# Kernel tuning notes

Hardware: AMD Instinct MI355X
Metric: run time of the kernel (lower is better)

The kernel has to match this reference:

```python
import jax, jax.numpy as jnp
import numpy as np

_EPSILON = 1e-06


def _allocation(usage):
    """Freeness-based allocation: sort usage, exclusive cumprod, scatter back.

    usage: [B, M] in [0, 1]. Returns allocation weights [B, M].
    """
    usage = _EPSILON + (1.0 - _EPSILON) * usage
    nonusage = 1.0 - usage
    m = usage.shape[-1]
    sorted_nonusage, indices = jax.lax.top_k(nonusage, k=m)  # descending nonusage = ascending usage
    sorted_usage = 1.0 - sorted_nonusage
    # exclusive cumulative product along the sorted memory axis
    prod_sorted_usage = jnp.concatenate(
        [jnp.ones_like(sorted_usage[:, :1]),
         jnp.cumprod(sorted_usage, axis=1)[:, :-1]], axis=1)
    sorted_allocation = sorted_nonusage * prod_sorted_usage
    # invert the permutation and gather back to original slot order
    inverse_indices = jnp.argsort(indices, axis=1)
    return jnp.take_along_axis(sorted_allocation, inverse_indices, axis=1)


def _updated_usage(write_weights, free_gate, read_weights, prev_usage):
    """Freeness.__call__: usage after write then after read/free. [B, M]."""
    ww = jax.lax.stop_gradient(write_weights)
    # usage after write: increase toward 1 at written slots
    write_w = 1.0 - jnp.prod(1.0 - ww, axis=1)          # [B, M]
    usage = prev_usage + (1.0 - prev_usage) * write_w
    # usage after read: decrease where free_gate*read_weights is high
    free_read = free_gate[:, :, None] * read_weights      # [B, R, M]
    phi = jnp.prod(1.0 - free_read, axis=1)               # [B, M]
    return usage * phi


def _write_allocation_weights(usage, write_gates, num_writes):
    """Per-write-head allocation weights. Returns [B, num_writes, M]."""
    wg = write_gates[:, :, None]                          # [B, W, 1]
    allocs = []
    for i in range(num_writes):  # small fixed head count; sequential by construction
        a = _allocation(usage)
        allocs.append(a)
        usage = usage + (1.0 - usage) * wg[:, i, :] * a
    return jnp.stack(allocs, axis=1)


def setup_inputs() -> dict:
    key = jax.random.key(0)
    ks = jax.random.split(key, 5)
    B, W, R, M = 512, 4, 8, 16384
    return {
        "write_weights": jax.random.uniform(ks[0], (B, W, M), dtype=jnp.float32),
        "free_gate": jax.random.uniform(ks[1], (B, R), dtype=jnp.float32),
        "read_weights": jax.random.uniform(ks[2], (B, R, M), dtype=jnp.float32),
        "prev_usage": jax.random.uniform(ks[3], (B, M), dtype=jnp.float32),
        "write_gates": jax.random.uniform(ks[4], (B, W), dtype=jnp.float32),
        "num_writes": W,
    }


def reference(write_weights, free_gate, read_weights, prev_usage, write_gates, num_writes):
    usage = _updated_usage(write_weights, free_gate, read_weights, prev_usage)
    alloc = _write_allocation_weights(usage, write_gates, num_writes)
    return usage, alloc
```

## Files before the change

### kernel.cpp

```cpp
#include <hip/hip_runtime.h>
#include <stdint.h>

typedef unsigned long long u64;
typedef unsigned int u32;
typedef unsigned short u16;
typedef float f32x4 __attribute__((ext_vector_type(4)));

#define NBINS 512
#define CAP 256
#define POOLCAP 1024
#define LOG_CUT (-30.0f)
#define NT 1024
#define MWW 256

__device__ __forceinline__ int bucket_of(u32 nnbits) {
    u32 d = 0x3F800000u - nnbits;
    if (d == 0u) d = 1u;
    const int e = 31 - __builtin_clz(d);
    const u32 sub = (e >= 4) ? ((d >> (e - 4)) & 15u) : ((d << (4 - e)) & 15u);
    int v = (e << 4) | (int)sub;
    if (v > NBINS - 1) v = NBINS - 1;
    return (NBINS - 1) - v;
}

__device__ __forceinline__ void nt_store4(float* p, float4 v) {
    f32x4 nv;
    nv.x = v.x; nv.y = v.y; nv.z = v.z; nv.w = v.w;
    __builtin_nontemporal_store(nv, (f32x4*)p);
}

template <int TW, int TR>
__global__ __launch_bounds__(NT, 8)
void fused_kernel(const float* __restrict__ ww,
                  const float* __restrict__ fg,
                  const float* __restrict__ rw,
                  const float* __restrict__ prev,
                  const float* __restrict__ wgt,
                  float* __restrict__ out_usage,
                  float* __restrict__ out_alloc,
                  int B, int W, int R, int M)
{
    __shared__ u64   poolKey[POOLCAP];
    __shared__ float poolLg[POOLCAP];
    __shared__ u64   candKey[CAP];
    __shared__ float candLg[CAP];
    __shared__ u16   candPos[CAP];
    __shared__ float sPart[3][CAP];
    __shared__ u32   hC[NBINS];
    __shared__ float mB[NBINS];
    __shared__ u32   tc[16];
    __shared__ float twv[16];
    __shared__ int   misc[6];
    __shared__ u64   bmS[TW > 0 ? TW : 1][MWW];
    __shared__ u32   boS[TW > 0 ? TW : 1][MWW];
    __shared__ float valS[TW > 0 ? TW : 1][CAP];

    const int Wl = TW > 0 ? TW : W;
    const int Rl = TR > 0 ? TR : R;
    const int b = blockIdx.x;
    const int t = threadIdx.x;
    const int lane = t & 63;
    const int wid = t >> 6;

    const float C1 = (float)(1.0 - 1e-6);
    const float CE = 1e-6f;
    const size_t rowOff = (size_t)b * M;

    if (t < NBINS) {
        hC[t] = 0u;
        const int v = NBINS - 1 - t;
        const int e = v >> 4;
        const u32 sub = (u32)(v & 15);
        const int sh = e >= 4 ? e - 4 : 0;
        u64 dhi64 = ((u64)(17u + sub) << sh) + 1u;
        u32 dhi = dhi64 > 0x3F800000ull ? 0x3F800000u : (u32)dhi64;
        const float nnlo = __uint_as_float(0x3F800000u - dhi);
        float ueub = 1.0f - nnlo;
        ueub = ueub < 1e-38f ? 1e-38f : (ueub > 0.9999999f ? 0.9999999f : ueub);
        mB[t] = __log2f(ueub);
    }
    if (TW > 0 && t < TW * MWW) bmS[t >> 8][t & (MWW - 1)] = 0ull;
    if (t == 0) { misc[0] = 0; misc[3] = NBINS; }
    __syncthreads();

    {
        float frs[TR > 0 ? TR : 8];
        #pragma unroll
        for (int r = 0; r < Rl; ++r) frs[r] = fg[(size_t)b * Rl + r];

        for (int m = t * 4; m < M; m += NT * 4) {
            const float4 pv = *(const float4*)(prev + rowOff + m);
            float pr0 = 1.f, pr1 = 1.f, pr2 = 1.f, pr3 = 1.f;
            #pragma unroll
            for (int w = 0; w < Wl; ++w) {
                const float4 a = *(const float4*)(ww + ((size_t)b * Wl + w) * M + m);
                pr0 *= (1.0f - a.x); pr1 *= (1.0f - a.y);
                pr2 *= (1.0f - a.z); pr3 *= (1.0f - a.w);
            }
            float u0 = pv.x + (1.0f - pv.x) * (1.0f - pr0);
            float u1 = pv.y + (1.0f - pv.y) * (1.0f - pr1);
            float u2 = pv.z + (1.0f - pv.z) * (1.0f - pr2);
            float u3 = pv.w + (1.0f - pv.w) * (1.0f - pr3);
            float f0 = 1.f, f1 = 1.f, f2 = 1.f, f3 = 1.f;
            #pragma unroll
            for (int r = 0; r < Rl; ++r) {
                const float fr = frs[r];
                const float4 a = *(const float4*)(rw + ((size_t)b * Rl + r) * M + m);
                f0 *= (1.0f - fr * a.x); f1 *= (1.0f - fr * a.y);
                f2 *= (1.0f - fr * a.z); f3 *= (1.0f - fr * a.w);
            }
            float4 uo;
            uo.x = u0 * f0; uo.y = u1 * f1; uo.z = u2 * f2; uo.w = u3 * f3;
            *(float4*)(out_usage + rowOff + m) = uo;
            if (TW == 0) {
                const float4 z = make_float4(0.f, 0.f, 0.f, 0.f);
                for (int w = 0; w < Wl; ++w)
                    nt_store4(out_alloc + ((size_t)b * Wl + w) * M + m, z);
            }
            const float ua[4] = {uo.x, uo.y, uo.z, uo.w};
            #pragma unroll
            for (int j = 0; j < 4; ++j) {
                const float nn = 1.0f - (CE + C1 * ua[j]);
                atomicAdd(&hC[bucket_of(__float_as_uint(nn))], 1u);
            }
        }
    }
    __syncthreads();

    {
        const bool act = (t < NBINS);
        u32 sc = 0; int x = 0;
        if (act) {
            x = NBINS - 1 - t;
            sc = hC[x];
            #pragma unroll
            for (int off = 1; off < 64; off <<= 1) {
                const u32 oc = __shfl_up(sc, off);
                if (lane >= off) sc += oc;
            }
            if (lane == 63) tc[wid] = sc;
        }
        __syncthreads();
        if (act) {
            u32 ac = 0;
            for (int q = 0; q < wid; ++q) ac += tc[q];
            sc += ac;
            if (sc <= (u32)POOLCAP) atomicMin(&misc[3], x);
        }
    }
    __syncthreads();
    const int pc = misc[3];

    for (int m = t * 4; m < M; m += NT * 4) {
        const float4 uu = *(const float4*)(out_usage + rowOff + m);
        const float ua[4] = {uu.x, uu.y, uu.z, uu.w};
        #pragma unroll
        for (int j = 0; j < 4; ++j) {
            const float ue = CE + C1 * ua[j];
            const float nn = 1.0f - ue;
            const u32 nnbits = __float_as_uint(nn);
            const int bkt = bucket_of(nnbits);
            const bool pred = (bkt >= pc) && (pc < NBINS);
            const u64 mask = __ballot(pred);
            const int cnt = __popcll(mask);
            if (cnt) {
                int base = 0;
                if (lane == 0) base = atomicAdd(&misc[0], cnt);
                base = __shfl(base, 0);
                if (pred) {
                    const int pos = base + __popcll(mask & ((1ull << lane) - 1));
                    if (pos < POOLCAP) {
                        poolKey[pos] = (((u64)(~nnbits)) << 16) | (u64)(u32)(m + j);
                        poolLg[pos] = __log2f(ue);
                    }
                }
            }
        }
    }
    __syncthreads();
    int P = misc[0]; if (P > POOLCAP) P = POOLCAP;

    for (int i = 0; i < Wl; ++i) {
        const float wgi = wgt[(size_t)b * Wl + i];
        float* orow = out_alloc + ((size_t)b * Wl + i) * M;

        if (t == 0) { misc[4] = 0; misc[1] = -1; misc[2] = NBINS; }
        __syncthreads();

        {
            const bool act = (t < NBINS);
            u32 sc = 0; float sw = 0.f; int x = 0;
            if (act) {
                x = NBINS - 1 - t;
                const u32 c = hC[x];
                sc = c;
                sw = mB[x] * (float)c;
                #pragma unroll
                for (int off = 1; off < 64; off <<= 1) {
                    const u32  oc = __shfl_up(sc, off);
                    const float ow = __shfl_up(sw, off);
                    if (lane >= off) { sc += oc; sw += ow; }
                }
                if (lane == 63) { tc[wid] = sc; twv[wid] = sw; }
            }
            __syncthreads();
            if (act) {
                u32 ac = 0; float aw = 0.f;
                for (int q = 0; q < wid; ++q) { ac += tc[q]; aw += twv[q]; }
                sc += ac; sw += aw;
                if (x >= pc) {
                    if (sw <= LOG_CUT) atomicMax(&misc[1], x);
                    if (sc <= (u32)CAP) atomicMin(&misc[2], x);
                }
            }
        }
        __syncthreads();
        const int xs = misc[1];
        const int xc = misc[2];
        const int cut = (xs > xc) ? xs : xc;

        if (t < P) {
            const u64 key = poolKey[t];
            const u32 nnbits = ~((u32)(key >> 16));
            const int bkt = bucket_of(nnbits);
            const bool pred = (bkt >= cut) && (cut < NBINS);
            const u64 mask = __ballot(pred);
            const int cnt = __popcll(mask);
            if (cnt) {
                int base = 0;
                if (lane == 0) base = atomicAdd(&misc[4], cnt);
                base = __shfl(base, 0);
                if (pred) {
                    const int pos = base + __popcll(mask & ((1ull << lane) - 1));
                    if (pos < CAP) {
                        candKey[pos] = key;
                        candLg[pos] = poolLg[t];
                        candPos[pos] = (u16)t;
                    }
                }
            }
        }
        __syncthreads();
        int K = misc[4]; if (K > CAP) K = CAP;

        const int c = t & (CAP - 1);
        const int g = t >> 8;
        float Sp = 0.0f;
        if (c < K) {
            const u64 mykey = candKey[c];
            const int k0 = (K * g) >> 2;
            const int k1 = (K * (g + 1)) >> 2;
            for (int k = k0; k < k1; ++k) {
                if (candKey[k] < mykey) Sp += candLg[k];
            }
        }
        if (g > 0) sPart[g - 1][c] = Sp;
        __syncthreads();

        float myAl = 0.0f; int myIdx = -1;
        if (t < K) {
            const float S = Sp + sPart[0][t] + sPart[1][t] + sPart[2][t];
            const u64 mykey = candKey[t];
            const u32 nnbits = ~((u32)(mykey >> 16));
            const float nn = __uint_as_float(nnbits);
            const int idx = (int)(mykey & 0xFFFFull);
            const float al = nn * __builtin_exp2f(S);
            if (al != 0.0f) {
                if (TW > 0) {
                    myAl = al; myIdx = idx;
                    atomicOr(&bmS[i][idx >> 6], 1ull << (idx & 63));
                } else {
                    orow[idx] = al;
                }
                if (i + 1 < Wl) {
                    const float ucur = (1.0f - nn - CE) / C1;
                    const float unew = ucur + ((1.0f - ucur) * wgi) * al;
                    const float nn2 = 1.0f - (CE + C1 * unew);
                    const u32 nn2bits = __float_as_uint(nn2);
                    const int p = (int)candPos[t];
                    poolKey[p] = (((u64)(~nn2bits)) << 16) | (u64)(u32)idx;
                    poolLg[p] = __log2f(1.0f - nn2);
                    const int bold = bucket_of(nnbits);
                    const int bnew = bucket_of(nn2bits);
                    if (bnew != bold) {
                        atomicSub(&hC[bold], 1u);
                        atomicAdd(&hC[bnew], 1u);
                    }
                }
            }
        }
        if (TW > 0) {
            __syncthreads();
            u32 myinc = 0, mycnt = 0;
            if (t < MWW) {
                mycnt = (u32)__popcll(bmS[i][t]);
                myinc = mycnt;
                #pragma unroll
                for (int off = 1; off < 64; off <<= 1) {
                    const u32 o = __shfl_up(myinc, off);
                    if (lane >= off) myinc += o;
                }
                if (lane == 63) tc[wid] = myinc;
            }
            __syncthreads();
            if (t < MWW) {
                u32 add = 0;
                for (int q = 0; q < wid; ++q) add += tc[q];
                boS[i][t] = myinc + add - mycnt;
            }
            __syncthreads();
            if (myIdx >= 0) {
                const u64 wb = bmS[i][myIdx >> 6];
                const int xr = (int)boS[i][myIdx >> 6]
                             + (int)__popcll(wb & ((1ull << (myIdx & 63)) - 1));
                valS[i][xr] = myAl;
            }
        }
        __syncthreads();
    }

    if (TW > 0) {
        for (int m4 = t * 4; m4 < M; m4 += NT * 4) {
            const int word = m4 >> 6;
            const int bit0 = m4 & 63;
            #pragma unroll
            for (int w = 0; w < TW; ++w) {
                const u64 wb = bmS[w][word];
                float4 o = make_float4(0.f, 0.f, 0.f, 0.f);
                if ((wb >> bit0) & 15ull) {
                    int base = (int)boS[w][word]
                             + (int)__popcll(wb & ((1ull << bit0) - 1));
                    float* op = &o.x;
                    #pragma unroll
                    for (int j = 0; j < 4; ++j) {
                        if ((wb >> (bit0 + j)) & 1ull) op[j] = valS[w][base++];
                    }
                }
                nt_store4(out_alloc + ((size_t)b * TW + w) * M + m4, o);
            }
        }
    }
}

extern "C" void kernel_launch(void* const* d_in, const int* in_sizes, int n_in,
                              void* d_out, int out_size, void* d_ws, size_t ws_size,
                              hipStream_t stream) {
    const float* ww   = (const float*)d_in[0];
    const float* fg   = (const float*)d_in[1];
    const float* rw   = (const float*)d_in[2];
    const float* prev = (const float*)d_in[3];
    const float* wgt  = (const float*)d_in[4];
    const int BWM = in_sizes[0];
    const int BR  = in_sizes[1];
    const int BM  = in_sizes[3];
    const int BW  = in_sizes[4];
    const int M = BWM / BW;
    const int B = BM / M;
    const int W = BW / B;
    const int R = BR / B;

    float* out_usage = (float*)d_out;
    float* out_alloc = out_usage + (size_t)BM;

    if (W == 4 && R == 8 && M == 16384) {
        hipLaunchKernelGGL((fused_kernel<4, 8>), dim3(B), dim3(NT), 0, stream,
                           ww, fg, rw, prev, wgt, out_usage, out_alloc, B, W, R, M);
    } else {
        hipLaunchKernelGGL((fused_kernel<0, 0>), dim3(B), dim3(NT), 0, stream,
                           ww, fg, rw, prev, wgt, out_usage, out_alloc, B, W, R, M);
    }
}
```

Measured before the change: 143.7 us.

## Cut block barriers with single-wave histogram scans and deferred bitmap compaction

Replaces the 512-thread multi-wave histogram scans (which needed extra barriers and shared atomics) with a single-wave scan where each lane covers 8 bins, followed by a wave-wide min/max reduction. The per-head bitmap prefix-sum compaction is moved out of the write-head loop and done once for all heads after it, with each thread keeping its per-head values in registers. The candidate rank loop now runs over a fixed CAP with sentinel keys instead of a variable count. Together these remove several __syncthreads per head in exchange for some redundant fixed-size comparison work and extra register use.

```diff
diff --git a/kernel.cpp b/kernel.cpp
--- a/kernel.cpp
+++ b/kernel.cpp
@@ -27,6 +27,45 @@
     f32x4 nv;
     nv.x = v.x; nv.y = v.y; nv.z = v.z; nv.w = v.w;
     __builtin_nontemporal_store(nv, (f32x4*)p);
+}
+
+__device__ __forceinline__ void wave0_scan(const u32* hC, const float* mB,
+                                           int gate, u32 capv, bool wantXs,
+                                           int* outXs, int* outXc, int lane) {
+    const int x0 = NBINS - 8 * (lane + 1);
+    u32 csum = 0; float wsum = 0.f;
+    #pragma unroll
+    for (int j = 0; j < 8; ++j) {
+        const u32 c = hC[x0 + j];
+        csum += c; wsum += mB[x0 + j] * (float)c;
+    }
+    u32 ics = csum; float iws = wsum;
+    #pragma unroll
+    for (int off = 1; off < 64; off <<= 1) {
+        const u32 oc = __shfl_up(ics, off);
+        const float ow = __shfl_up(iws, off);
+        if (lane >= off) { ics += oc; iws += ow; }
+    }
+    u32 rc = ics - csum; float rw = iws - wsum;
+    int myxs = -1, myxc = NBINS;
+    #pragma unroll
+    for (int j = 7; j >= 0; --j) {
+        const int x = x0 + j;
+        const u32 c = hC[x];
+        rc += c; rw += mB[x] * (float)c;
+        if (x >= gate) {
+            if (wantXs && rw <= LOG_CUT && x > myxs) myxs = x;
+            if (rc <= capv && x < myxc) myxc = x;
+        }
+    }
+    #pragma unroll
+    for (int off = 1; off < 64; off <<= 1) {
+        const int oxs = __shfl_xor(myxs, off);
+        const int oxc = __shfl_xor(myxc, off);
+        if (oxs > myxs) myxs = oxs;
+        if (oxc < myxc) myxc = oxc;
+    }
+    if (lane == 0) { *outXs = myxs; *outXc = myxc; }
 }
 
 template <int TW, int TR>
@@ -48,8 +87,7 @@
     __shared__ float sPart[3][CAP];
     __shared__ u32   hC[NBINS];
     __shared__ float mB[NBINS];
-    __shared__ u32   tc[16];
-    __shared__ float twv[16];
+    __shared__ u32   wvS[16];
     __shared__ int   misc[6];
     __shared__ u64   bmS[TW > 0 ? TW : 1][MWW];
     __shared__ u32   boS[TW > 0 ? TW : 1][MWW];
@@ -80,7 +118,7 @@
         mB[t] = __log2f(ueub);
     }
     if (TW > 0 && t < TW * MWW) bmS[t >> 8][t & (MWW - 1)] = 0ull;
-    if (t == 0) { misc[0] = 0; misc[3] = NBINS; }
+    if (t == 0) { misc[0] = 0; misc[3] = NBINS; misc[4] = 0; }
     __syncthreads();
 
     {
@@ -127,27 +165,7 @@
     }
     __syncthreads();
 
-    {
-        const bool act = (t < NBINS);
-        u32 sc = 0; int x = 0;
-        if (act) {
-            x = NBINS - 1 - t;
-            sc = hC[x];
-            #pragma unroll
-            for (int off = 1; off < 64; off <<= 1) {
-                const u32 oc = __shfl_up(sc, off);
-                if (lane >= off) sc += oc;
-            }
-            if (lane == 63) tc[wid] = sc;
-        }
-        __syncthreads();
-        if (act) {
-            u32 ac = 0;
-            for (int q = 0; q < wid; ++q) ac += tc[q];
-            sc += ac;
-            if (sc <= (u32)POOLCAP) atomicMin(&misc[3], x);
-        }
-    }
+    if (wid == 0) wave0_scan(hC, mB, 0, (u32)POOLCAP, false, &misc[1], &misc[3], lane);
     __syncthreads();
     const int pc = misc[3];
 
@@ -180,40 +198,19 @@
     __syncthreads();
     int P = misc[0]; if (P > POOLCAP) P = POOLCAP;
 
+    float myAl[TW > 0 ? TW : 1];
+    int   myIdx[TW > 0 ? TW : 1];
+    #pragma unroll
+    for (int i = 0; i < (TW > 0 ? TW : 1); ++i) myIdx[i] = -1;
+
+    #pragma unroll
     for (int i = 0; i < Wl; ++i) {
         const float wgi = wgt[(size_t)b * Wl + i];
         float* orow = out_alloc + ((size_t)b * Wl + i) * M;
 
-        if (t == 0) { misc[4] = 0; misc[1] = -1; misc[2] = NBINS; }
-        __syncthreads();
-
-        {
-            const bool act = (t < NBINS);
-            u32 sc = 0; float sw = 0.f; int x = 0;
-            if (act) {
-                x = NBINS - 1 - t;
-                const u32 c = hC[x];
-                sc = c;
-                sw = mB[x] * (float)c;
-                #pragma unroll
-                for (int off = 1; off < 64; off <<= 1) {
-                    const u32  oc = __shfl_up(sc, off);
-                    const float ow = __shfl_up(sw, off);
-                    if (lane >= off) { sc += oc; sw += ow; }
-                }
-                if (lane == 63) { tc[wid] = sc; twv[wid] = sw; }
-            }
-            __syncthreads();
-            if (act) {
-                u32 ac = 0; float aw = 0.f;
-                for (int q = 0; q < wid; ++q) { ac += tc[q]; aw += twv[q]; }
-                sc += ac; sw += aw;
-                if (x >= pc) {
-                    if (sw <= LOG_CUT) atomicMax(&misc[1], x);
-                    if (sc <= (u32)CAP) atomicMin(&misc[2], x);
-                }
-            }
-        }
+        if (wid == 0) wave0_scan(hC, mB, pc, (u32)CAP, true, &misc[1], &misc[2], lane);
+        if (t >= 256 && t < 256 + CAP) candKey[t - 256] = ~0ull;
+        if (t == 576) misc[4] = 0;
         __syncthreads();
         const int xs = misc[1];
         const int xc = misc[2];
@@ -241,33 +238,30 @@
             }
         }
         __syncthreads();
-        int K = misc[4]; if (K > CAP) K = CAP;
 
         const int c = t & (CAP - 1);
         const int g = t >> 8;
+        const u64 mykey = candKey[c];
         float Sp = 0.0f;
-        if (c < K) {
-            const u64 mykey = candKey[c];
-            const int k0 = (K * g) >> 2;
-            const int k1 = (K * (g + 1)) >> 2;
-            for (int k = k0; k < k1; ++k) {
+        {
+            const int k0 = g * (CAP / 4);
+            #pragma unroll 4
+            for (int k = k0; k < k0 + CAP / 4; ++k) {
                 if (candKey[k] < mykey) Sp += candLg[k];
             }
         }
         if (g > 0) sPart[g - 1][c] = Sp;
         __syncthreads();
 
-        float myAl = 0.0f; int myIdx = -1;
-        if (t < K) {
+        if (t < CAP && mykey != ~0ull) {
             const float S = Sp + sPart[0][t] + sPart[1][t] + sPart[2][t];
-            const u64 mykey = candKey[t];
             const u32 nnbits = ~((u32)(mykey >> 16));
             const float nn = __uint_as_float(nnbits);
             const int idx = (int)(mykey & 0xFFFFull);
             const float al = nn * __builtin_exp2f(S);
             if (al != 0.0f) {
                 if (TW > 0) {
-                    myAl = al; myIdx = idx;
+                    myAl[i] = al; myIdx[i] = idx;
                     atomicOr(&bmS[i][idx >> 6], 1ull << (idx & 63));
                 } else {
                     orow[idx] = al;
@@ -289,54 +283,56 @@
                 }
             }
         }
-        if (TW > 0) {
-            __syncthreads();
-            u32 myinc = 0, mycnt = 0;
-            if (t < MWW) {
-                mycnt = (u32)__popcll(bmS[i][t]);
-                myinc = mycnt;
-                #pragma unroll
-                for (int off = 1; off < 64; off <<= 1) {
-                    const u32 o = __shfl_up(myinc, off);
-                    if (lane >= off) myinc += o;
-                }
-                if (lane == 63) tc[wid] = myinc;
-            }
-            __syncthreads();
-            if (t < MWW) {
-                u32 add = 0;
-                for (int q = 0; q < wid; ++q) add += tc[q];
-                boS[i][t] = myinc + add - mycnt;
-            }
-            __syncthreads();
-            if (myIdx >= 0) {
-                const u64 wb = bmS[i][myIdx >> 6];
-                const int xr = (int)boS[i][myIdx >> 6]
-                             + (int)__popcll(wb & ((1ull << (myIdx & 63)) - 1));
-                valS[i][xr] = myAl;
-            }
-        }
         __syncthreads();
     }
 
     if (TW > 0) {
+        const int h = t >> 8;
+        const int w = t & (MWW - 1);
+        const u32 mycnt = (u32)__popcll(bmS[h][w]);
+        u32 inc = mycnt;
+        #pragma unroll
+        for (int off = 1; off < 64; off <<= 1) {
+            const u32 o = __shfl_up(inc, off);
+            if (lane >= off) inc += o;
+        }
+        if (lane == 63) wvS[wid] = inc;
+        __syncthreads();
+        {
+            u32 add = 0;
+            const int w0 = h * 4;
+            for (int q = w0; q < wid; ++q) add += wvS[q];
+            boS[h][w] = add + inc - mycnt;
+        }
+        __syncthreads();
+        #pragma unroll
+        for (int i = 0; i < TW; ++i) {
+            if (myIdx[i] >= 0) {
+                const u64 wb = bmS[i][myIdx[i] >> 6];
+                const int xr = (int)boS[i][myIdx[i] >> 6]
+                             + (int)__popcll(wb & ((1ull << (myIdx[i] & 63)) - 1));
+                valS[i][xr] = myAl[i];
+            }
+        }
+        __syncthreads();
+
         for (int m4 = t * 4; m4 < M; m4 += NT * 4) {
             const int word = m4 >> 6;
             const int bit0 = m4 & 63;
             #pragma unroll
-            for (int w = 0; w < TW; ++w) {
-                const u64 wb = bmS[w][word];
+            for (int w2 = 0; w2 < TW; ++w2) {
+                const u64 wb = bmS[w2][word];
                 float4 o = make_float4(0.f, 0.f, 0.f, 0.f);
                 if ((wb >> bit0) & 15ull) {
-                    int base = (int)boS[w][word]
+                    int base = (int)boS[w2][word]
                              + (int)__popcll(wb & ((1ull << bit0) - 1));
                     float* op = &o.x;
                     #pragma unroll
                     for (int j = 0; j < 4; ++j) {
-                        if ((wb >> (bit0 + j)) & 1ull) op[j] = valS[w][base++];
+                        if ((wb >> (bit0 + j)) & 1ull) op[j] = valS[w2][base++];
                     }
                 }
-                nt_store4(out_alloc + ((size_t)b * TW + w) * M + m4, o);
+                nt_store4(out_alloc + ((size_t)b * TW + w2) * M + m4, o);
             }
         }
     }
```

Measured after the change: 149.7 us. 4.2% more time.
